# Performance work log

Hardware: AMD Instinct MI355X
Metric: run time of the kernel (lower is better)

The kernel has to match this reference:

```python
import jax, jax.numpy as jnp
import numpy as np

N_NODES = 50000
N_EDGES = 800000
NODE_DIM = 32
EDGE_DIM = 16
HIDDEN = 64


def setup_inputs() -> dict:
    key = jax.random.key(0)
    ks = jax.random.split(key, 7)
    h = jax.random.normal(ks[0], (N_NODES, HIDDEN), dtype=jnp.float32)
    nf = jax.random.normal(ks[1], (N_NODES, NODE_DIM), dtype=jnp.float32)
    ef = jax.random.normal(ks[2], (N_EDGES, EDGE_DIM), dtype=jnp.float32)
    src = jax.random.randint(ks[3], (N_EDGES,), 0, N_NODES, dtype=jnp.int32)
    dst = jax.random.randint(ks[4], (N_EDGES,), 0, N_NODES, dtype=jnp.int32)
    # torch Linear weights: [out_features, in_features]
    in1 = HIDDEN + 2 * NODE_DIM + EDGE_DIM  # 144
    W1 = jax.random.normal(ks[5], (HIDDEN, in1), dtype=jnp.float32) * (1.0 / np.sqrt(in1))
    W2 = jax.random.normal(ks[6], (HIDDEN, HIDDEN), dtype=jnp.float32) * (1.0 / np.sqrt(HIDDEN))
    return {"h": h, "nf": nf, "ef": ef, "src": src, "dst": dst, "W1": W1, "W2": W2}


def reference(h, nf, ef, src, dst, W1, W2):
    n = nf.shape[0]
    # per-edge message: concat(dst.x, edge.x, src.h)  -> [E, node+edge+hidden]
    m_e = jnp.concatenate([nf[dst], ef, h[src]], axis=-1)
    # mailbox sum per destination node
    m = jax.ops.segment_sum(m_e, dst, num_segments=n)  # [N, node+edge+hidden]
    z = jnp.concatenate([nf, m], axis=-1)              # [N, hidden+2*node+edge]
    new_h = jax.nn.relu(z @ W1.T) @ W2.T               # [N, hidden]
    # DGL update_all only updates nodes that received at least one message
    deg = jax.ops.segment_sum(jnp.ones_like(dst, dtype=jnp.float32), dst, num_segments=n)
    return jnp.where(deg[:, None] > 0, new_h, h)
```

## Files before the change

kernel.cpp:

```cpp
#include <hip/hip_runtime.h>

#define NDIM 32
#define EDIM 16
#define NHID 64
#define NIN1 144
#define SCHUNK 1024
#define SPT 4

__global__ __launch_bounds__(256) void sse_hist(
    const int* __restrict__ dst, int* __restrict__ counts,
    const float* __restrict__ W1, float* __restrict__ W1T,
    const float* __restrict__ W2, float* __restrict__ W2T, int E) {
  int e = blockIdx.x * 256 + threadIdx.x;
  if (e < NHID * NIN1) {
    int r = e / NIN1, k = e - r * NIN1;
    W1T[k * NHID + r] = W1[e];
  } else if (e < NHID * NIN1 + NHID * NHID) {
    int i = e - NHID * NIN1;
    int r = i >> 6, k = i & 63;
    W2T[k * NHID + r] = W2[i];
  }
  if (e < E) atomicAdd(&counts[dst[e]], 1);
}

__global__ __launch_bounds__(256) void sse_scan_part(
    const int* __restrict__ counts, int* __restrict__ bsum, int N) {
  __shared__ int ws[4];
  int t = threadIdx.x;
  int base = blockIdx.x * SCHUNK + t * SPT;
  int s = 0;
#pragma unroll
  for (int i = 0; i < SPT; ++i) {
    int idx = base + i;
    if (idx < N) s += counts[idx];
  }
  int v = s;
#pragma unroll
  for (int off = 1; off < 64; off <<= 1) v += __shfl_xor(v, off, 64);
  if ((t & 63) == 0) ws[t >> 6] = v;
  __syncthreads();
  if (t == 0) bsum[blockIdx.x] = ws[0] + ws[1] + ws[2] + ws[3];
}

__global__ __launch_bounds__(256) void sse_scan_final(
    const int* __restrict__ counts, const int* __restrict__ bsum,
    int* __restrict__ starts, int* __restrict__ cursors, int N, int nb) {
  __shared__ int ws[4];
  int t = threadIdx.x;
  int lane = t & 63, w = t >> 6;
  int boff = 0;
  for (int j = 0; j < (int)blockIdx.x; ++j) boff += bsum[j];
  int base = blockIdx.x * SCHUNK + t * SPT;
  int c[SPT];
  int s = 0;
#pragma unroll
  for (int i = 0; i < SPT; ++i) {
    int idx = base + i;
    c[i] = (idx < N) ? counts[idx] : 0;
    s += c[i];
  }
  int incl = s;
#pragma unroll
  for (int off = 1; off < 64; off <<= 1) {
    int u = __shfl_up(incl, off, 64);
    if (lane >= off) incl += u;
  }
  if (lane == 63) ws[w] = incl;
  __syncthreads();
  int woff = 0;
#pragma unroll
  for (int j = 0; j < 4; ++j)
    if (j < w) woff += ws[j];
  int run = boff + woff + (incl - s);
#pragma unroll
  for (int i = 0; i < SPT; ++i) {
    int idx = base + i;
    if (idx < N) {
      starts[idx] = run;
      cursors[idx] = run;
      run += c[i];
    }
  }
  if ((int)blockIdx.x == nb - 1 && t == 0)
    starts[N] = boff + ws[0] + ws[1] + ws[2] + ws[3];
}

__global__ __launch_bounds__(256) void sse_build(
    const int* __restrict__ src, const int* __restrict__ dst,
    int* __restrict__ cursors, int2* __restrict__ sedge, int E) {
  int e = blockIdx.x * 256 + threadIdx.x;
  if (e >= E) return;
  int d = dst[e];
  int pos = atomicAdd(&cursors[d], 1);
  sedge[pos] = make_int2(src[e], e);
}

__global__ __launch_bounds__(256) void sse_gather(
    const float* __restrict__ h, const float* __restrict__ ef,
    const int* __restrict__ starts, const int2* __restrict__ sedge,
    float* __restrict__ efsum, float* __restrict__ hsum, int N) {
  int node = blockIdx.x * 4 + (threadIdx.x >> 6);
  int lane = threadIdx.x & 63;
  if (node >= N) return;
  int st = starts[node], en = starts[node + 1];
  const float4* h4 = (const float4*)h;
  const float4* ef4 = (const float4*)ef;

  int q = lane >> 4, m = lane & 15;
  float4 ha = make_float4(0.f, 0.f, 0.f, 0.f);
  int j = st;
  for (; j + 7 < en; j += 8) {
    int s0 = sedge[j + q].x;
    int s1 = sedge[j + 4 + q].x;
    float4 v0 = h4[(size_t)s0 * 16 + m];
    float4 v1 = h4[(size_t)s1 * 16 + m];
    ha.x += v0.x + v1.x;
    ha.y += v0.y + v1.y;
    ha.z += v0.z + v1.z;
    ha.w += v0.w + v1.w;
  }
  if (j + 3 < en) {
    int s0 = sedge[j + q].x;
    float4 v0 = h4[(size_t)s0 * 16 + m];
    ha.x += v0.x; ha.y += v0.y; ha.z += v0.z; ha.w += v0.w;
    j += 4;
  }
  if (j + q < en) {
    int s0 = sedge[j + q].x;
    float4 v0 = h4[(size_t)s0 * 16 + m];
    ha.x += v0.x; ha.y += v0.y; ha.z += v0.z; ha.w += v0.w;
  }
#pragma unroll
  for (int off = 16; off < 64; off <<= 1) {
    ha.x += __shfl_xor(ha.x, off, 64);
    ha.y += __shfl_xor(ha.y, off, 64);
    ha.z += __shfl_xor(ha.z, off, 64);
    ha.w += __shfl_xor(ha.w, off, 64);
  }
  if (lane < 16) ((float4*)hsum)[(size_t)node * 16 + m] = ha;

  int eq = lane >> 2, em = lane & 3;
  float4 ea = make_float4(0.f, 0.f, 0.f, 0.f);
  for (j = st; j + 15 < en; j += 16) {
    int eid = sedge[j + eq].y;
    float4 v = ef4[(size_t)eid * 4 + em];
    ea.x += v.x; ea.y += v.y; ea.z += v.z; ea.w += v.w;
  }
  if (j + eq < en) {
    int eid = sedge[j + eq].y;
    float4 v = ef4[(size_t)eid * 4 + em];
    ea.x += v.x; ea.y += v.y; ea.z += v.z; ea.w += v.w;
  }
#pragma unroll
  for (int off = 4; off < 64; off <<= 1) {
    ea.x += __shfl_xor(ea.x, off, 64);
    ea.y += __shfl_xor(ea.y, off, 64);
    ea.z += __shfl_xor(ea.z, off, 64);
    ea.w += __shfl_xor(ea.w, off, 64);
  }
  if (lane < 4) ((float4*)efsum)[(size_t)node * 4 + em] = ea;
}

__global__ __launch_bounds__(256) void sse_node(
    const float* __restrict__ h, const float* __restrict__ nf,
    const float* __restrict__ efsum, const float* __restrict__ hsum,
    const int* __restrict__ starts, const float* __restrict__ W1T,
    const float* __restrict__ W2T, float* __restrict__ out, int N) {
  __shared__ float4 zs[36 * 64];
  __shared__ float4 as[16 * 64];

  int tid = threadIdx.x;
  int lane = tid & 63;
  int w = __builtin_amdgcn_readfirstlane(tid) >> 6;

  int node = blockIdx.x * 64 + lane;
  int nodeC = node < N ? node : N - 1;

  if (w == 0) {
    int st = starts[nodeC], en = starts[nodeC + 1];
    float dg = (float)(en - st);
    const float4* nfr = (const float4*)(nf + (size_t)nodeC * NDIM);
#pragma unroll
    for (int k4 = 0; k4 < 8; ++k4) {
      float4 v = nfr[k4];
      zs[k4 * 64 + lane] = v;
      zs[(8 + k4) * 64 + lane] =
          make_float4(dg * v.x, dg * v.y, dg * v.z, dg * v.w);
    }
  } else if (w == 1) {
    const float4* efr = (const float4*)(efsum + (size_t)nodeC * EDIM);
#pragma unroll
    for (int k4 = 0; k4 < 4; ++k4) zs[(16 + k4) * 64 + lane] = efr[k4];
  } else if (w == 2) {
    const float4* hsr = (const float4*)(hsum + (size_t)nodeC * NHID);
#pragma unroll
    for (int k4 = 0; k4 < 8; ++k4) zs[(20 + k4) * 64 + lane] = hsr[k4];
  } else {
    const float4* hsr = (const float4*)(hsum + (size_t)nodeC * NHID);
#pragma unroll
    for (int k4 = 8; k4 < 16; ++k4) zs[(20 + k4) * 64 + lane] = hsr[k4];
  }
  __syncthreads();

  const float4* w1b = (const float4*)W1T + w * 4;
  float a[16];
#pragma unroll
  for (int j = 0; j < 16; ++j) a[j] = 0.f;

#pragma unroll 2
  for (int k4 = 0; k4 < 36; ++k4) {
    float4 zv = zs[k4 * 64 + lane];
#pragma unroll
    for (int kk = 0; kk < 4; ++kk) {
      int k = k4 * 4 + kk;
      float4 w0 = w1b[k * 16 + 0];
      float4 w1 = w1b[k * 16 + 1];
      float4 w2 = w1b[k * 16 + 2];
      float4 w3 = w1b[k * 16 + 3];
      float zk = kk == 0 ? zv.x : kk == 1 ? zv.y : kk == 2 ? zv.z : zv.w;
      a[0]  = fmaf(w0.x, zk, a[0]);
      a[1]  = fmaf(w0.y, zk, a[1]);
      a[2]  = fmaf(w0.z, zk, a[2]);
      a[3]  = fmaf(w0.w, zk, a[3]);
      a[4]  = fmaf(w1.x, zk, a[4]);
      a[5]  = fmaf(w1.y, zk, a[5]);
      a[6]  = fmaf(w1.z, zk, a[6]);
      a[7]  = fmaf(w1.w, zk, a[7]);
      a[8]  = fmaf(w2.x, zk, a[8]);
      a[9]  = fmaf(w2.y, zk, a[9]);
      a[10] = fmaf(w2.z, zk, a[10]);
      a[11] = fmaf(w2.w, zk, a[11]);
      a[12] = fmaf(w3.x, zk, a[12]);
      a[13] = fmaf(w3.y, zk, a[13]);
      a[14] = fmaf(w3.z, zk, a[14]);
      a[15] = fmaf(w3.w, zk, a[15]);
    }
  }

#pragma unroll
  for (int j4 = 0; j4 < 4; ++j4)
    as[(w * 4 + j4) * 64 + lane] =
        make_float4(fmaxf(a[j4 * 4 + 0], 0.f), fmaxf(a[j4 * 4 + 1], 0.f),
                    fmaxf(a[j4 * 4 + 2], 0.f), fmaxf(a[j4 * 4 + 3], 0.f));
  __syncthreads();

  const float4* w2b = (const float4*)W2T + w * 4;
  float o[16];
#pragma unroll
  for (int j = 0; j < 16; ++j) o[j] = 0.f;

#pragma unroll 2
  for (int kq = 0; kq < 16; ++kq) {
    float4 av = as[kq * 64 + lane];
#pragma unroll
    for (int kk = 0; kk < 4; ++kk) {
      int k = kq * 4 + kk;
      float4 w0 = w2b[k * 16 + 0];
      float4 w1 = w2b[k * 16 + 1];
      float4 w2 = w2b[k * 16 + 2];
      float4 w3 = w2b[k * 16 + 3];
      float ak = kk == 0 ? av.x : kk == 1 ? av.y : kk == 2 ? av.z : av.w;
      o[0]  = fmaf(w0.x, ak, o[0]);
      o[1]  = fmaf(w0.y, ak, o[1]);
      o[2]  = fmaf(w0.z, ak, o[2]);
      o[3]  = fmaf(w0.w, ak, o[3]);
      o[4]  = fmaf(w1.x, ak, o[4]);
      o[5]  = fmaf(w1.y, ak, o[5]);
      o[6]  = fmaf(w1.z, ak, o[6]);
      o[7]  = fmaf(w1.w, ak, o[7]);
      o[8]  = fmaf(w2.x, ak, o[8]);
      o[9]  = fmaf(w2.y, ak, o[9]);
      o[10] = fmaf(w2.z, ak, o[10]);
      o[11] = fmaf(w2.w, ak, o[11]);
      o[12] = fmaf(w3.x, ak, o[12]);
      o[13] = fmaf(w3.y, ak, o[13]);
      o[14] = fmaf(w3.z, ak, o[14]);
      o[15] = fmaf(w3.w, ak, o[15]);
    }
  }

  if (node < N) {
    int st = starts[node], en = starts[node + 1];
    float4* o4 = (float4*)(out + (size_t)node * NHID + w * 16);
    if (en - st == 0) {
      const float4* hr = (const float4*)(h + (size_t)node * NHID + w * 16);
#pragma unroll
      for (int j4 = 0; j4 < 4; ++j4) o4[j4] = hr[j4];
    } else {
#pragma unroll
      for (int j4 = 0; j4 < 4; ++j4)
        o4[j4] = make_float4(o[j4 * 4 + 0], o[j4 * 4 + 1], o[j4 * 4 + 2],
                             o[j4 * 4 + 3]);
    }
  }
}

extern "C" void kernel_launch(void* const* d_in, const int* in_sizes, int n_in,
                              void* d_out, int out_size, void* d_ws, size_t ws_size,
                              hipStream_t stream) {
  const float* h  = (const float*)d_in[0];
  const float* nf = (const float*)d_in[1];
  const float* ef = (const float*)d_in[2];
  const int*   src = (const int*)d_in[3];
  const int*   dst = (const int*)d_in[4];
  const float* W1 = (const float*)d_in[5];
  const float* W2 = (const float*)d_in[6];
  float* out = (float*)d_out;

  int N = in_sizes[0] / NHID;
  int E = in_sizes[3];

  char* p = (char*)d_ws;
  int2* sedge = (int2*)p;                 p += (size_t)E * 8;
  int* counts = (int*)p;                  p += (size_t)N * 4;
  int* starts = (int*)p;                  p += (size_t)(N + 1) * 4;
  int* cursors = (int*)p;                 p += (size_t)N * 4;
  int* bsum = (int*)p;                    p += 64 * 4;
  float* W1T = (float*)p;                 p += (size_t)NIN1 * NHID * 4;
  float* W2T = (float*)p;                 p += (size_t)NHID * NHID * 4;
  p = (char*)(((size_t)p + 15) & ~(size_t)15);
  float* efsum = (float*)p;               p += (size_t)N * EDIM * 4;
  float* hsum = (float*)p;

  hipMemsetAsync(counts, 0, (size_t)N * sizeof(int), stream);

  int eblocks = (E + 255) / 256;
  int nb = (N + SCHUNK - 1) / SCHUNK;

  sse_hist<<<eblocks, 256, 0, stream>>>(dst, counts, W1, W1T, W2, W2T, E);
  sse_scan_part<<<nb, 256, 0, stream>>>(counts, bsum, N);
  sse_scan_final<<<nb, 256, 0, stream>>>(counts, bsum, starts, cursors, N, nb);
  sse_build<<<eblocks, 256, 0, stream>>>(src, dst, cursors, sedge, E);

  int gblocks = (N + 3) / 4;
  sse_gather<<<gblocks, 256, 0, stream>>>(h, ef, starts, sedge, efsum, hsum, N);

  int nblocks = (N + 63) / 64;
  sse_node<<<nblocks, 256, 0, stream>>>(h, nf, efsum, hsum, starts, W1T, W2T,
                                        out, N);
}
```

Baseline: 273.1 us.

## Fuse neighbor gather into node MLP kernel and store only edge ids

Merges the per-node gather of h and ef sums into the MLP kernel, writing the sums directly into shared memory instead of round-tripping hsum/efsum through global memory. The sorted edge list now stores only the edge id, with src looked up indirectly, which halves the build write traffic. The risk is lower parallelism in the gather: each wave now walks 16 nodes serially in a block of 64 nodes, compared with one node per wave before, and the extra src indirection adds a dependent load.

```diff
diff --git a/kernel.cpp b/kernel.cpp
--- a/kernel.cpp
+++ b/kernel.cpp
@@ -86,119 +86,97 @@
 }
 
 __global__ __launch_bounds__(256) void sse_build(
-    const int* __restrict__ src, const int* __restrict__ dst,
-    int* __restrict__ cursors, int2* __restrict__ sedge, int E) {
+    const int* __restrict__ dst, int* __restrict__ cursors,
+    int* __restrict__ seid, int E) {
   int e = blockIdx.x * 256 + threadIdx.x;
   if (e >= E) return;
-  int d = dst[e];
-  int pos = atomicAdd(&cursors[d], 1);
-  sedge[pos] = make_int2(src[e], e);
-}
-
-__global__ __launch_bounds__(256) void sse_gather(
-    const float* __restrict__ h, const float* __restrict__ ef,
-    const int* __restrict__ starts, const int2* __restrict__ sedge,
-    float* __restrict__ efsum, float* __restrict__ hsum, int N) {
-  int node = blockIdx.x * 4 + (threadIdx.x >> 6);
-  int lane = threadIdx.x & 63;
-  if (node >= N) return;
-  int st = starts[node], en = starts[node + 1];
-  const float4* h4 = (const float4*)h;
-  const float4* ef4 = (const float4*)ef;
-
-  int q = lane >> 4, m = lane & 15;
-  float4 ha = make_float4(0.f, 0.f, 0.f, 0.f);
-  int j = st;
-  for (; j + 7 < en; j += 8) {
-    int s0 = sedge[j + q].x;
-    int s1 = sedge[j + 4 + q].x;
-    float4 v0 = h4[(size_t)s0 * 16 + m];
-    float4 v1 = h4[(size_t)s1 * 16 + m];
-    ha.x += v0.x + v1.x;
-    ha.y += v0.y + v1.y;
-    ha.z += v0.z + v1.z;
-    ha.w += v0.w + v1.w;
-  }
-  if (j + 3 < en) {
-    int s0 = sedge[j + q].x;
-    float4 v0 = h4[(size_t)s0 * 16 + m];
-    ha.x += v0.x; ha.y += v0.y; ha.z += v0.z; ha.w += v0.w;
-    j += 4;
-  }
-  if (j + q < en) {
-    int s0 = sedge[j + q].x;
-    float4 v0 = h4[(size_t)s0 * 16 + m];
-    ha.x += v0.x; ha.y += v0.y; ha.z += v0.z; ha.w += v0.w;
-  }
-#pragma unroll
-  for (int off = 16; off < 64; off <<= 1) {
-    ha.x += __shfl_xor(ha.x, off, 64);
-    ha.y += __shfl_xor(ha.y, off, 64);
-    ha.z += __shfl_xor(ha.z, off, 64);
-    ha.w += __shfl_xor(ha.w, off, 64);
-  }
-  if (lane < 16) ((float4*)hsum)[(size_t)node * 16 + m] = ha;
-
-  int eq = lane >> 2, em = lane & 3;
-  float4 ea = make_float4(0.f, 0.f, 0.f, 0.f);
-  for (j = st; j + 15 < en; j += 16) {
-    int eid = sedge[j + eq].y;
-    float4 v = ef4[(size_t)eid * 4 + em];
-    ea.x += v.x; ea.y += v.y; ea.z += v.z; ea.w += v.w;
-  }
-  if (j + eq < en) {
-    int eid = sedge[j + eq].y;
-    float4 v = ef4[(size_t)eid * 4 + em];
-    ea.x += v.x; ea.y += v.y; ea.z += v.z; ea.w += v.w;
-  }
-#pragma unroll
-  for (int off = 4; off < 64; off <<= 1) {
-    ea.x += __shfl_xor(ea.x, off, 64);
-    ea.y += __shfl_xor(ea.y, off, 64);
-    ea.z += __shfl_xor(ea.z, off, 64);
-    ea.w += __shfl_xor(ea.w, off, 64);
-  }
-  if (lane < 4) ((float4*)efsum)[(size_t)node * 4 + em] = ea;
-}
-
-__global__ __launch_bounds__(256) void sse_node(
+  int pos = atomicAdd(&cursors[dst[e]], 1);
+  seid[pos] = e;
+}
+
+__global__ __launch_bounds__(256) void sse_fused(
     const float* __restrict__ h, const float* __restrict__ nf,
-    const float* __restrict__ efsum, const float* __restrict__ hsum,
-    const int* __restrict__ starts, const float* __restrict__ W1T,
-    const float* __restrict__ W2T, float* __restrict__ out, int N) {
+    const float* __restrict__ ef, const int* __restrict__ src,
+    const int* __restrict__ starts, const int* __restrict__ seid,
+    const float* __restrict__ W1T, const float* __restrict__ W2T,
+    float* __restrict__ out, int N) {
   __shared__ float4 zs[36 * 64];
-  __shared__ float4 as[16 * 64];
 
   int tid = threadIdx.x;
   int lane = tid & 63;
   int w = __builtin_amdgcn_readfirstlane(tid) >> 6;
-
-  int node = blockIdx.x * 64 + lane;
-  int nodeC = node < N ? node : N - 1;
-
-  if (w == 0) {
-    int st = starts[nodeC], en = starts[nodeC + 1];
-    float dg = (float)(en - st);
-    const float4* nfr = (const float4*)(nf + (size_t)nodeC * NDIM);
-#pragma unroll
-    for (int k4 = 0; k4 < 8; ++k4) {
-      float4 v = nfr[k4];
-      zs[k4 * 64 + lane] = v;
-      zs[(8 + k4) * 64 + lane] =
-          make_float4(dg * v.x, dg * v.y, dg * v.z, dg * v.w);
-    }
-  } else if (w == 1) {
-    const float4* efr = (const float4*)(efsum + (size_t)nodeC * EDIM);
-#pragma unroll
-    for (int k4 = 0; k4 < 4; ++k4) zs[(16 + k4) * 64 + lane] = efr[k4];
-  } else if (w == 2) {
-    const float4* hsr = (const float4*)(hsum + (size_t)nodeC * NHID);
-#pragma unroll
-    for (int k4 = 0; k4 < 8; ++k4) zs[(20 + k4) * 64 + lane] = hsr[k4];
-  } else {
-    const float4* hsr = (const float4*)(hsum + (size_t)nodeC * NHID);
-#pragma unroll
-    for (int k4 = 8; k4 < 16; ++k4) zs[(20 + k4) * 64 + lane] = hsr[k4];
+  int nbase = blockIdx.x * 64;
+
+  for (int i = tid; i < 512; i += 256) {
+    int nl = i >> 3, k4 = i & 7;
+    int n = nbase + nl;
+    int nC = n < N ? n : N - 1;
+    float dg = (float)(starts[nC + 1] - starts[nC]);
+    float4 v = ((const float4*)(nf + (size_t)nC * NDIM))[k4];
+    zs[k4 * 64 + nl] = v;
+    zs[(8 + k4) * 64 + nl] = make_float4(dg * v.x, dg * v.y, dg * v.z, dg * v.w);
+  }
+
+  const float4* h4 = (const float4*)h;
+  const float4* ef4 = (const float4*)ef;
+  int q = lane >> 4, m = lane & 15;
+  int eq = lane >> 2, em = lane & 3;
+  for (int nl = w * 16; nl < w * 16 + 16; ++nl) {
+    int n = nbase + nl;
+    if (n >= N) break;
+    int st = starts[n], en = starts[n + 1];
+
+    float4 ha = make_float4(0.f, 0.f, 0.f, 0.f);
+    int j = st;
+    for (; j + 7 < en; j += 8) {
+      int e0 = seid[j + q], e1 = seid[j + 4 + q];
+      int s0 = src[e0], s1 = src[e1];
+      float4 v0 = h4[(size_t)s0 * 16 + m];
+      float4 v1 = h4[(size_t)s1 * 16 + m];
+      ha.x += v0.x + v1.x;
+      ha.y += v0.y + v1.y;
+      ha.z += v0.z + v1.z;
+      ha.w += v0.w + v1.w;
+    }
+    if (j + 3 < en) {
+      int s0 = src[seid[j + q]];
+      float4 v0 = h4[(size_t)s0 * 16 + m];
+      ha.x += v0.x; ha.y += v0.y; ha.z += v0.z; ha.w += v0.w;
+      j += 4;
+    }
+    if (j + q < en) {
+      int s0 = src[seid[j + q]];
+      float4 v0 = h4[(size_t)s0 * 16 + m];
+      ha.x += v0.x; ha.y += v0.y; ha.z += v0.z; ha.w += v0.w;
+    }
+#pragma unroll
+    for (int off = 16; off < 64; off <<= 1) {
+      ha.x += __shfl_xor(ha.x, off, 64);
+      ha.y += __shfl_xor(ha.y, off, 64);
+      ha.z += __shfl_xor(ha.z, off, 64);
+      ha.w += __shfl_xor(ha.w, off, 64);
+    }
+    if (lane < 16) zs[(20 + m) * 64 + nl] = ha;
+
+    float4 ea = make_float4(0.f, 0.f, 0.f, 0.f);
+    for (j = st; j + 15 < en; j += 16) {
+      int eid = seid[j + eq];
+      float4 v = ef4[(size_t)eid * 4 + em];
+      ea.x += v.x; ea.y += v.y; ea.z += v.z; ea.w += v.w;
+    }
+    if (j + eq < en) {
+      int eid = seid[j + eq];
+      float4 v = ef4[(size_t)eid * 4 + em];
+      ea.x += v.x; ea.y += v.y; ea.z += v.z; ea.w += v.w;
+    }
+#pragma unroll
+    for (int off = 4; off < 64; off <<= 1) {
+      ea.x += __shfl_xor(ea.x, off, 64);
+      ea.y += __shfl_xor(ea.y, off, 64);
+      ea.z += __shfl_xor(ea.z, off, 64);
+      ea.w += __shfl_xor(ea.w, off, 64);
+    }
+    if (lane < 4) zs[(16 + em) * 64 + nl] = ea;
   }
   __syncthreads();
 
@@ -236,7 +214,9 @@
       a[15] = fmaf(w3.w, zk, a[15]);
     }
   }
-
+  __syncthreads();
+
+  float4* as = zs;
 #pragma unroll
   for (int j4 = 0; j4 < 4; ++j4)
     as[(w * 4 + j4) * 64 + lane] =
@@ -279,6 +259,7 @@
     }
   }
 
+  int node = nbase + lane;
   if (node < N) {
     int st = starts[node], en = starts[node + 1];
     float4* o4 = (float4*)(out + (size_t)node * NHID + w * 16);
@@ -311,16 +292,13 @@
   int E = in_sizes[3];
 
   char* p = (char*)d_ws;
-  int2* sedge = (int2*)p;                 p += (size_t)E * 8;
+  int* seid = (int*)p;                    p += (size_t)E * 4;
   int* counts = (int*)p;                  p += (size_t)N * 4;
   int* starts = (int*)p;                  p += (size_t)(N + 1) * 4;
   int* cursors = (int*)p;                 p += (size_t)N * 4;
   int* bsum = (int*)p;                    p += 64 * 4;
   float* W1T = (float*)p;                 p += (size_t)NIN1 * NHID * 4;
-  float* W2T = (float*)p;                 p += (size_t)NHID * NHID * 4;
-  p = (char*)(((size_t)p + 15) & ~(size_t)15);
-  float* efsum = (float*)p;               p += (size_t)N * EDIM * 4;
-  float* hsum = (float*)p;
+  float* W2T = (float*)p;
 
   hipMemsetAsync(counts, 0, (size_t)N * sizeof(int), stream);
 
@@ -330,12 +308,9 @@
   sse_hist<<<eblocks, 256, 0, stream>>>(dst, counts, W1, W1T, W2, W2T, E);
   sse_scan_part<<<nb, 256, 0, stream>>>(counts, bsum, N);
   sse_scan_final<<<nb, 256, 0, stream>>>(counts, bsum, starts, cursors, N, nb);
-  sse_build<<<eblocks, 256, 0, stream>>>(src, dst, cursors, sedge, E);
-
-  int gblocks = (N + 3) / 4;
-  sse_gather<<<gblocks, 256, 0, stream>>>(h, ef, starts, sedge, efsum, hsum, N);
+  sse_build<<<eblocks, 256, 0, stream>>>(dst, cursors, seid, E);
 
   int nblocks = (N + 63) / 64;
-  sse_node<<<nblocks, 256, 0, stream>>>(h, nf, efsum, hsum, starts, W1T, W2T,
-                                        out, N);
-}
+  sse_fused<<<nblocks, 256, 0, stream>>>(h, nf, ef, src, starts, seid,
+                                         W1T, W2T, out, N);
+}
```

Result: slower. 290.7 us (+6.4%).
